# Optimization experiments

Hardware: AMD Instinct MI355X
Metric: run time of the kernel (lower is better)

The kernel has to match this reference:

```python
import jax, jax.numpy as jnp
import numpy as np

Q_SCALE = 64  # 1 << 6, from quantize_8bit default
Q_STEP = 2.0 / Q_SCALE
Q_MIN = -(2 ** 7) / Q_SCALE      # -128/64 = -2.0
Q_MAX = (2 ** 7 - 1) / Q_SCALE   # 127/64


def quantize_8bit(x):
    # round-to-step with straight-through estimator (matches slayer quantize), then clamp
    xq = x + jax.lax.stop_gradient(jnp.round(x / Q_STEP) * Q_STEP - x)
    return jnp.clip(xq, Q_MIN, Q_MAX)


def weight_norm(v, g):
    # per-output-channel weight norm: w = g * v / ||v||  (v: [out, in])
    n = jnp.sqrt(jnp.sum(v * v, axis=1, keepdims=True))
    return g[:, None] * v / n


def sigma_delta_block(x, v, g, clamp6):
    # x: [N, Cin, H, W, T]
    qw = quantize_8bit(weight_norm(v, g))           # [Cout, Cin], 8-bit quantized
    y = jnp.einsum('oi,nihwt->nohwt', qw, x)        # 1x1x1 conv (pointwise)
    s = jnp.cumsum(y, axis=-1)                      # sigma unit: accumulate over time
    mean = jnp.mean(s, axis=(0, 2, 3, 4), keepdims=True)  # mean-only batchnorm
    a = s - mean
    if clamp6:                                      # Clamp6 activation (fc2); Ind = identity (fc1)
        a = jnp.clip(a, -6.0, 6.0)
    # delta unit, threshold=0: d[t] = a[t] - a[t-1], a[-1] = 0
    d = jnp.diff(a, axis=-1, prepend=jnp.zeros_like(a[..., :1]))
    return d


def setup_inputs() -> dict:
    key = jax.random.key(0)
    k = jax.random.split(key, 5)
    N, C, H, W, T = 4, 128, 32, 32, 32
    Cs = 32
    x = jax.random.normal(k[0], (N, C, H, W, T), dtype=jnp.float32)
    v1 = jax.random.normal(k[1], (Cs, C), dtype=jnp.float32) * 0.1
    g1 = jax.random.uniform(k[2], (Cs,), dtype=jnp.float32) + 0.5
    v2 = jax.random.normal(k[3], (C, Cs), dtype=jnp.float32) * 0.1
    g2 = jax.random.uniform(k[4], (C,), dtype=jnp.float32) + 0.5
    return {'x': x, 'v1': v1, 'g1': g1, 'v2': v2, 'g2': g2}


def reference(x, v1, g1, v2, g2):
    h = sigma_delta_block(x, v1, g1, clamp6=False)   # fc1: Ind activation
    out = sigma_delta_block(h, v2, g2, clamp6=True)  # fc2: Clamp6 activation
    return out
```

## Files before the change

kernel.cpp:

```cpp
#include <hip/hip_runtime.h>

#define CIN  128
#define CHUNKF 32768

typedef float f32x4 __attribute__((ext_vector_type(4)));
typedef short s16x8 __attribute__((ext_vector_type(8)));


__device__ __forceinline__ uint pack_hilo(float f) {
  uint b = __float_as_uint(f);
  uint hi = b & 0xffff0000u;
  float lo = f - __uint_as_float(hi);
  return (hi >> 16) | (__float_as_uint(lo) & 0xffff0000u);
}

__global__ __launch_bounds__(256) void wnorm_mean_kernel(
    const float* __restrict__ x,
    const float* __restrict__ v1, const float* __restrict__ g1,
    const float* __restrict__ v2, const float* __restrict__ g2,
    float* __restrict__ ws) {
  int tid = threadIdx.x;
  if (blockIdx.x < 2048) {
    int b = blockIdx.x;
    int chunk = b >> 2, quarter = b & 3;
    int i = chunk & 127;
    const float4* xp = (const float4*)(x + (size_t)chunk * CHUNKF + (size_t)quarter * 8192);
    float acc = 0.f;
#pragma unroll
    for (int it = 0; it < 8; ++it) {
      int f4i = tid + 256 * it;
      float4 v = xp[f4i];
      int t0 = (4 * f4i) & 31;
      acc += v.x * (float)(32 - t0) + v.y * (float)(31 - t0)
           + v.z * (float)(30 - t0) + v.w * (float)(29 - t0);
    }
    for (int off = 32; off >= 1; off >>= 1) acc += __shfl_down(acc, off);
    __shared__ float part[4];
    if ((tid & 63) == 0) part[tid >> 6] = acc;
    __syncthreads();
    if (tid == 0) atomicAdd(&ws[8192 + i], part[0] + part[1] + part[2] + part[3]);
  } else {
    int b = blockIdx.x - 2048;
    bool first = (b < 32);
    int row = first ? b : b - 32;
    int len = first ? 128 : 32;
    const float* v = first ? v1 : v2;
    const float* g = first ? g1 : g2;

    double val = 0.0;
    if (tid < len) { double t = (double)v[row * len + tid]; val = t * t; }
    for (int off = 32; off >= 1; off >>= 1) val += __shfl_down(val, off);
    __shared__ double partial[4];
    if ((tid & 63) == 0) partial[tid >> 6] = val;
    __syncthreads();
    double norm = sqrt(partial[0] + partial[1]);
    if (tid < len) {
      double w = (double)g[row] * (double)v[row * len + tid] / norm;
      double qd = rint(w * 32.0) * 0.03125;
      qd = fmin(fmax(qd, -2.0), 1.984375);
      float qf = (float)qd;
      ushort bf = (ushort)(__float_as_uint(qf) >> 16);
      if (first) {
        ws[row * 128 + tid] = qf;
        ((ushort*)(ws + 8448))[row * 128 + tid] = bf;
      } else {
        ws[4096 + row * 32 + tid] = qf;
        ((ushort*)(ws + 10496))[row * 32 + tid] = bf;
      }
    }
  }
}

__global__ __launch_bounds__(256, 4) void fused_kernel(
    const float* __restrict__ x, const float* __restrict__ ws,
    float* __restrict__ out) {
  const ushort* qw1bf = (const ushort*)(ws + 8448);
  const ushort* qw2bf = (const ushort*)(ws + 10496);

  __shared__ uint xs[8192];
  __shared__ float zred[288];
  __shared__ float kls[128];

  const int tid = threadIdx.x;
  const int wv = tid >> 6;
  const int l  = tid & 63;
  const int g  = l >> 4;
  const int ln = l & 15;

  const int nb  = blockIdx.x >> 8;
  const int hw0 = (blockIdx.x & 255) * 4;
  const float* xblk = x + (size_t)nb * CIN * CHUNKF + (size_t)hw0 * 32;

  float4 xr[8];
#pragma unroll
  for (int k = 0; k < 8; ++k) {
    int f = k * 256 + tid, c = f >> 5, n4 = f & 31;
    xr[k] = *(const float4*)(xblk + (size_t)c * CHUNKF + n4 * 4);
  }

  s16x8 A1[2][4];
#pragma unroll
  for (int jt = 0; jt < 2; ++jt)
#pragma unroll
    for (int ks = 0; ks < 4; ++ks)
      A1[jt][ks] = *(const s16x8*)(qw1bf + (jt * 16 + ln) * 128 + ks * 32 + g * 8);

  {
    int j = tid & 31, grp = tid >> 5;
    const float* qr = ws + j * 128 + grp * 16;
    const float* mr = ws + 8192 + grp * 16;
    float pp = 0.f;
#pragma unroll
    for (int cc = 0; cc < 16; ++cc) pp += qr[cc] * mr[cc];
    zred[j * 8 + grp] = pp;
  }
  __syncthreads();
  if (tid < 32) {
    float t = 0.f;
#pragma unroll
    for (int gg = 0; gg < 8; ++gg) t += zred[tid * 8 + gg];
    zred[256 + tid] = t * (1.0f / 131072.0f);
  }
  __syncthreads();
  if (tid < 128) {
    const float* q2 = ws + 4096 + tid * 32;
    float kk = 0.f;
#pragma unroll 8
    for (int j = 0; j < 32; ++j) kk += q2[j] * zred[256 + j];
    kls[tid] = kk;
  }

  f32x4 acc1[2][2];
#pragma unroll
  for (int a = 0; a < 2; ++a)
#pragma unroll
    for (int b = 0; b < 2; ++b) acc1[a][b] = (f32x4){0.f, 0.f, 0.f, 0.f};

#pragma unroll
  for (int ph = 0; ph < 2; ++ph) {
#pragma unroll
    for (int k = 0; k < 8; ++k) {
      int f = k * 256 + tid, c = f >> 5, n4 = f & 31;
      int u = n4 ^ ((c >> 2) & 6);
      uint4 pk;
      pk.x = pack_hilo(xr[k].x); pk.y = pack_hilo(xr[k].y);
      pk.z = pack_hilo(xr[k].z); pk.w = pack_hilo(xr[k].w);
      *(uint4*)&xs[c * 128 + u * 4] = pk;
    }
    __syncthreads();
    if (ph == 0) {
#pragma unroll
      for (int k = 0; k < 8; ++k) {
        int f = k * 256 + tid, c = f >> 5, n4 = f & 31;
        xr[k] = *(const float4*)(xblk + (size_t)(64 + c) * CHUNKF + n4 * 4);
      }
    }
#pragma unroll
    for (int kl = 0; kl < 2; ++kl) {
#pragma unroll
      for (int nt = 0; nt < 2; ++nt) {
        const int n = wv * 32 + nt * 16 + ln;
        uint q0, q1, q2, q3, q4, q5, q6, q7;
        {
          const int base = (kl * 32 + g * 8) * 128;
          const int u = ((n >> 2) ^ (((kl * 32 + g * 8) >> 2) & 6)) * 4 + (n & 3);
          q0 = xs[base + 0 * 128 + u]; q1 = xs[base + 1 * 128 + u];
          q2 = xs[base + 2 * 128 + u]; q3 = xs[base + 3 * 128 + u];
          q4 = xs[base + 4 * 128 + u]; q5 = xs[base + 5 * 128 + u];
          q6 = xs[base + 6 * 128 + u]; q7 = xs[base + 7 * 128 + u];
        }
        uint4 H, L;
        H.x = (q0 & 0xffffu) | (q1 << 16);  H.y = (q2 & 0xffffu) | (q3 << 16);
        H.z = (q4 & 0xffffu) | (q5 << 16);  H.w = (q6 & 0xffffu) | (q7 << 16);
        L.x = (q0 >> 16) | (q1 & 0xffff0000u); L.y = (q2 >> 16) | (q3 & 0xffff0000u);
        L.z = (q4 >> 16) | (q5 & 0xffff0000u); L.w = (q6 >> 16) | (q7 & 0xffff0000u);
        s16x8 Bh = __builtin_bit_cast(s16x8, H);
        s16x8 Bl = __builtin_bit_cast(s16x8, L);
#pragma unroll
        for (int jt = 0; jt < 2; ++jt) {
          acc1[jt][nt] = __builtin_amdgcn_mfma_f32_16x16x32_bf16(
              A1[jt][ph * 2 + kl], Bh, acc1[jt][nt], 0, 0, 0);
          acc1[jt][nt] = __builtin_amdgcn_mfma_f32_16x16x32_bf16(
              A1[jt][ph * 2 + kl], Bl, acc1[jt][nt], 0, 0, 0);
        }
      }
    }
    __syncthreads();
  }

  uint* zw = xs + wv * 1024;
#pragma unroll
  for (int jt = 0; jt < 2; ++jt)
#pragma unroll
    for (int nt = 0; nt < 2; ++nt) {
      int n = nt * 16 + ln;
      int u = (jt * 4 + g) ^ (n & 7);
      uint4 pk;
      pk.x = pack_hilo(acc1[jt][nt][0]);
      pk.y = pack_hilo(acc1[jt][nt][1]);
      pk.z = pack_hilo(acc1[jt][nt][2]);
      pk.w = pack_hilo(acc1[jt][nt][3]);
      *(uint4*)&zw[n * 32 + u * 4] = pk;
    }

  s16x8 Ah[2], Al[2];
#pragma unroll
  for (int mt = 0; mt < 2; ++mt) {
    int n = mt * 16 + ln;
    int u0 = (2 * g) ^ (n & 7);
    int u1 = (2 * g + 1) ^ (n & 7);
    uint4 qa = *(const uint4*)&zw[n * 32 + u0 * 4];
    uint4 qb = *(const uint4*)&zw[n * 32 + u1 * 4];
    uint4 H, L;
    H.x = (qa.x & 0xffffu) | (qa.y << 16);  H.y = (qa.z & 0xffffu) | (qa.w << 16);
    H.z = (qb.x & 0xffffu) | (qb.y << 16);  H.w = (qb.z & 0xffffu) | (qb.w << 16);
    L.x = (qa.x >> 16) | (qa.y & 0xffff0000u); L.y = (qa.z >> 16) | (qa.w & 0xffff0000u);
    L.z = (qb.x >> 16) | (qb.y & 0xffff0000u); L.w = (qb.z >> 16) | (qb.w & 0xffff0000u);
    Ah[mt] = __builtin_bit_cast(s16x8, H);
    Al[mt] = __builtin_bit_cast(s16x8, L);
  }

  const size_t outbase = (size_t)nb * CIN * CHUNKF + (size_t)(hw0 + wv) * 32;
#pragma unroll 1
  for (int h = 0; h < 2; ++h) {
    s16x8 B2[4];
#pragma unroll
    for (int q = 0; q < 4; ++q)
      B2[q] = *(const s16x8*)(qw2bf + ((h * 4 + q) * 16 + ln) * 32 + g * 8);

    f32x4 acc2[4][2];
#pragma unroll
    for (int a = 0; a < 4; ++a)
#pragma unroll
      for (int b = 0; b < 2; ++b) acc2[a][b] = (f32x4){0.f, 0.f, 0.f, 0.f};

#pragma unroll
    for (int mt = 0; mt < 2; ++mt)
#pragma unroll
      for (int q = 0; q < 4; ++q) {
        acc2[q][mt] = __builtin_amdgcn_mfma_f32_16x16x32_bf16(Ah[mt], B2[q], acc2[q][mt], 0, 0, 0);
        acc2[q][mt] = __builtin_amdgcn_mfma_f32_16x16x32_bf16(Al[mt], B2[q], acc2[q][mt], 0, 0, 0);
      }

#pragma unroll
    for (int q = 0; q < 4; ++q) {
      const int nt = h * 4 + q;
      float c0[2], c1[2], c2[2], c3[2], base[2], Qi0 = 0.f;
#pragma unroll
      for (int mt = 0; mt < 2; ++mt) {
        c0[mt] = acc2[q][mt][0];
        c1[mt] = c0[mt] + acc2[q][mt][1];
        c2[mt] = c1[mt] + acc2[q][mt][2];
        c3[mt] = c2[mt] + acc2[q][mt][3];
        float Qi = c3[mt];
        float t1 = __shfl_up(Qi, 16); if (g >= 1) Qi += t1;
        float t2 = __shfl_up(Qi, 32); if (g >= 2) Qi += t2;
        base[mt] = Qi - c3[mt];
        if (mt == 0) Qi0 = Qi;
      }
      float S0tot = __shfl(Qi0, 48 + ln);
      base[1] += S0tot;
      const float kpp = kls[nt * 16 + ln];
      float* op = out + outbase + (size_t)(nt * 16 + ln) * CHUNKF;
#pragma unroll
      for (int mt = 0; mt < 2; ++mt) {
        float Bv = base[mt] - kpp;
        float prev = fminf(fmaxf(Bv, -6.f), 6.f);
        if (mt == 0 && g == 0) prev = 0.f;
        float A0 = fminf(fmaxf(Bv + c0[mt], -6.f), 6.f);
        float A1v = fminf(fmaxf(Bv + c1[mt], -6.f), 6.f);
        float A2v = fminf(fmaxf(Bv + c2[mt], -6.f), 6.f);
        float A3v = fminf(fmaxf(Bv + c3[mt], -6.f), 6.f);
        *(float4*)(op + mt * 16 + g * 4) =
            make_float4(A0 - prev, A1v - A0, A2v - A1v, A3v - A2v);
      }
    }
  }
}

extern "C" void kernel_launch(void* const* d_in, const int* in_sizes, int n_in,
                              void* d_out, int out_size, void* d_ws, size_t ws_size,
                              hipStream_t stream) {
  const float* x  = (const float*)d_in[0];
  const float* v1 = (const float*)d_in[1];
  const float* g1 = (const float*)d_in[2];
  const float* v2 = (const float*)d_in[3];
  const float* g2 = (const float*)d_in[4];
  float* ws  = (float*)d_ws;
  float* out = (float*)d_out;

  hipMemsetAsync(ws + 8192, 0, 128 * sizeof(float), stream);
  wnorm_mean_kernel<<<2208, 256, 0, stream>>>(x, v1, g1, v2, g2, ws);
  fused_kernel<<<1024, 256, 0, stream>>>(x, ws, out);
}
```

Measured before the change: 49.39 us.

## Fuse weight-norm, mean reduction and main pass into one cooperative kernel

Adds a cooperative kernel with 512 persistent blocks that first computes the time-weighted channel sums of its own x slice into 32 sharded atomic slots and quantizes the weights, then does a grid-wide sync and runs the two-GEMM sigma-delta pass over two 4-position groups, prefetching the next group's x into registers. It removes the separate pre-pass kernel launch and spreads the atomic contention across slots. In exchange it adds per-launch host queries for device attributes and occupancy, a grid barrier, and reads x twice within the same kernel. The old two-kernel path remains as a fallback when cooperative launch or the needed occupancy is unavailable.

Result: no change. 49.28 us (-0.2%).

```diff
diff --git a/kernel.cpp b/kernel.cpp
--- a/kernel.cpp
+++ b/kernel.cpp
@@ -1,4 +1,7 @@
 #include <hip/hip_runtime.h>
+#include <hip/hip_cooperative_groups.h>
+
+namespace cg = cooperative_groups;
 
 #define CIN  128
 #define CHUNKF 32768
@@ -46,7 +49,6 @@
     int len = first ? 128 : 32;
     const float* v = first ? v1 : v2;
     const float* g = first ? g1 : g2;
-
     double val = 0.0;
     if (tid < len) { double t = (double)v[row * len + tid]; val = t * t; }
     for (int off = 32; off >= 1; off >>= 1) val += __shfl_down(val, off);
@@ -160,15 +162,12 @@
 #pragma unroll
       for (int nt = 0; nt < 2; ++nt) {
         const int n = wv * 32 + nt * 16 + ln;
-        uint q0, q1, q2, q3, q4, q5, q6, q7;
-        {
-          const int base = (kl * 32 + g * 8) * 128;
-          const int u = ((n >> 2) ^ (((kl * 32 + g * 8) >> 2) & 6)) * 4 + (n & 3);
-          q0 = xs[base + 0 * 128 + u]; q1 = xs[base + 1 * 128 + u];
-          q2 = xs[base + 2 * 128 + u]; q3 = xs[base + 3 * 128 + u];
-          q4 = xs[base + 4 * 128 + u]; q5 = xs[base + 5 * 128 + u];
-          q6 = xs[base + 6 * 128 + u]; q7 = xs[base + 7 * 128 + u];
-        }
+        const int base = (kl * 32 + g * 8) * 128;
+        const int u = ((n >> 2) ^ (((kl * 32 + g * 8) >> 2) & 6)) * 4 + (n & 3);
+        uint q0 = xs[base + 0 * 128 + u], q1 = xs[base + 1 * 128 + u];
+        uint q2 = xs[base + 2 * 128 + u], q3 = xs[base + 3 * 128 + u];
+        uint q4 = xs[base + 4 * 128 + u], q5 = xs[base + 5 * 128 + u];
+        uint q6 = xs[base + 6 * 128 + u], q7 = xs[base + 7 * 128 + u];
         uint4 H, L;
         H.x = (q0 & 0xffffu) | (q1 << 16);  H.y = (q2 & 0xffffu) | (q3 << 16);
         H.z = (q4 & 0xffffu) | (q5 << 16);  H.w = (q6 & 0xffffu) | (q7 << 16);
@@ -178,10 +177,8 @@
         s16x8 Bl = __builtin_bit_cast(s16x8, L);
 #pragma unroll
         for (int jt = 0; jt < 2; ++jt) {
-          acc1[jt][nt] = __builtin_amdgcn_mfma_f32_16x16x32_bf16(
-              A1[jt][ph * 2 + kl], Bh, acc1[jt][nt], 0, 0, 0);
-          acc1[jt][nt] = __builtin_amdgcn_mfma_f32_16x16x32_bf16(
-              A1[jt][ph * 2 + kl], Bl, acc1[jt][nt], 0, 0, 0);
+          acc1[jt][nt] = __builtin_amdgcn_mfma_f32_16x16x32_bf16(A1[jt][ph * 2 + kl], Bh, acc1[jt][nt], 0, 0, 0);
+          acc1[jt][nt] = __builtin_amdgcn_mfma_f32_16x16x32_bf16(A1[jt][ph * 2 + kl], Bl, acc1[jt][nt], 0, 0, 0);
         }
       }
     }
@@ -227,13 +224,11 @@
 #pragma unroll
     for (int q = 0; q < 4; ++q)
       B2[q] = *(const s16x8*)(qw2bf + ((h * 4 + q) * 16 + ln) * 32 + g * 8);
-
     f32x4 acc2[4][2];
 #pragma unroll
     for (int a = 0; a < 4; ++a)
 #pragma unroll
       for (int b = 0; b < 2; ++b) acc2[a][b] = (f32x4){0.f, 0.f, 0.f, 0.f};
-
 #pragma unroll
     for (int mt = 0; mt < 2; ++mt)
 #pragma unroll
@@ -241,7 +236,6 @@
         acc2[q][mt] = __builtin_amdgcn_mfma_f32_16x16x32_bf16(Ah[mt], B2[q], acc2[q][mt], 0, 0, 0);
         acc2[q][mt] = __builtin_amdgcn_mfma_f32_16x16x32_bf16(Al[mt], B2[q], acc2[q][mt], 0, 0, 0);
       }
-
 #pragma unroll
     for (int q = 0; q < 4; ++q) {
       const int nt = h * 4 + q;
@@ -278,6 +272,288 @@
   }
 }
 
+__global__ __launch_bounds__(256, 2) void fused_all(
+    const float* __restrict__ x,
+    const float* __restrict__ v1, const float* __restrict__ g1,
+    const float* __restrict__ v2, const float* __restrict__ g2,
+    float* __restrict__ ws, float* __restrict__ out) {
+  __shared__ uint xs[8192];
+  __shared__ float mls[128];
+  __shared__ float zred[256];
+  __shared__ float zsm[32];
+  __shared__ float kls[128];
+  __shared__ double wpart[4];
+
+  const int tid = threadIdx.x;
+  const int bid = blockIdx.x;
+  const int nb  = bid >> 7;
+  const int hw8 = (bid & 127) * 8;
+  float* msumP = ws + 8192;
+
+  {
+    const int l63 = tid & 63, wvp = tid >> 6;
+    const int t0 = (4 * l63) & 31;
+    const float wt0 = (float)(32 - t0), wt1 = (float)(31 - t0);
+    const float wt2 = (float)(30 - t0), wt3 = (float)(29 - t0);
+    const int slot = bid & 31;
+    const float* xsl = x + (size_t)nb * CIN * CHUNKF + (size_t)hw8 * 32 + l63 * 4;
+#pragma unroll 4
+    for (int k = 0; k < 32; ++k) {
+      int c = k * 4 + wvp;
+      float4 v = *(const float4*)(xsl + (size_t)c * CHUNKF);
+      float pv = v.x * wt0 + v.y * wt1 + v.z * wt2 + v.w * wt3;
+      pv += __shfl_down(pv, 32);
+      pv += __shfl_down(pv, 16);
+      pv += __shfl_down(pv, 8);
+      pv += __shfl_down(pv, 4);
+      pv += __shfl_down(pv, 2);
+      pv += __shfl_down(pv, 1);
+      if (l63 == 0) atomicAdd(&msumP[slot * 128 + c], pv);
+    }
+  }
+
+  if (bid < 160) {
+    bool first = (bid < 32);
+    int row = first ? bid : bid - 32;
+    int len = first ? 128 : 32;
+    const float* v = first ? v1 : v2;
+    const float* g = first ? g1 : g2;
+    double val = 0.0;
+    if (tid < len) { double t = (double)v[row * len + tid]; val = t * t; }
+    for (int off = 32; off >= 1; off >>= 1) val += __shfl_down(val, off);
+    if ((tid & 63) == 0) wpart[tid >> 6] = val;
+    __syncthreads();
+    double norm = sqrt(wpart[0] + wpart[1]);
+    if (tid < len) {
+      double w = (double)g[row] * (double)v[row * len + tid] / norm;
+      double qd = rint(w * 32.0) * 0.03125;
+      qd = fmin(fmax(qd, -2.0), 1.984375);
+      float qf = (float)qd;
+      ushort bf = (ushort)(__float_as_uint(qf) >> 16);
+      if (first) {
+        ws[row * 128 + tid] = qf;
+        ((ushort*)(ws + 12544))[row * 128 + tid] = bf;
+      } else {
+        ws[4096 + row * 32 + tid] = qf;
+        ((ushort*)(ws + 14592))[row * 32 + tid] = bf;
+      }
+    }
+  }
+
+  cg::this_grid().sync();
+
+  const ushort* qw1bf = (const ushort*)(ws + 12544);
+  const ushort* qw2bf = (const ushort*)(ws + 14592);
+  const int wv = tid >> 6;
+  const int l  = tid & 63;
+  const int g  = l >> 4;
+  const int ln = l & 15;
+
+  s16x8 A1[2][4];
+#pragma unroll
+  for (int jt = 0; jt < 2; ++jt)
+#pragma unroll
+    for (int ks = 0; ks < 4; ++ks)
+      A1[jt][ks] = *(const s16x8*)(qw1bf + (jt * 16 + ln) * 128 + ks * 32 + g * 8);
+
+  float4 xr[8];
+  {
+    const float* xg = x + (size_t)nb * CIN * CHUNKF + (size_t)hw8 * 32;
+#pragma unroll
+    for (int k = 0; k < 8; ++k) {
+      int f = k * 256 + tid, c = f >> 5, n4 = f & 31;
+      xr[k] = *(const float4*)(xg + (size_t)c * CHUNKF + n4 * 4);
+    }
+  }
+
+  if (tid < 128) {
+    float m = 0.f;
+#pragma unroll
+    for (int p = 0; p < 32; ++p) m += msumP[p * 128 + tid];
+    mls[tid] = m;
+  }
+  __syncthreads();
+  {
+    int j = tid & 31, grp8 = tid >> 5;
+    const float* qr = ws + j * 128 + grp8 * 16;
+    float pp = 0.f;
+#pragma unroll
+    for (int cc = 0; cc < 16; ++cc) pp += qr[cc] * mls[grp8 * 16 + cc];
+    zred[j * 8 + grp8] = pp;
+  }
+  __syncthreads();
+  if (tid < 32) {
+    float t = 0.f;
+#pragma unroll
+    for (int gg = 0; gg < 8; ++gg) t += zred[tid * 8 + gg];
+    zsm[tid] = t * (1.0f / 131072.0f);
+  }
+  __syncthreads();
+  if (tid < 128) {
+    const float* q2p = ws + 4096 + tid * 32;
+    float kk = 0.f;
+#pragma unroll 8
+    for (int j = 0; j < 32; ++j) kk += q2p[j] * zsm[j];
+    kls[tid] = kk;
+  }
+
+#pragma unroll 1
+  for (int grp = 0; grp < 2; ++grp) {
+    const int hw0 = hw8 + grp * 4;
+    const float* xg = x + (size_t)nb * CIN * CHUNKF + (size_t)hw0 * 32;
+
+    f32x4 acc1[2][2];
+#pragma unroll
+    for (int a = 0; a < 2; ++a)
+#pragma unroll
+      for (int b = 0; b < 2; ++b) acc1[a][b] = (f32x4){0.f, 0.f, 0.f, 0.f};
+
+    __syncthreads();
+
+#pragma unroll
+    for (int ph = 0; ph < 2; ++ph) {
+#pragma unroll
+      for (int k = 0; k < 8; ++k) {
+        int f = k * 256 + tid, c = f >> 5, n4 = f & 31;
+        int u = n4 ^ ((c >> 2) & 6);
+        uint4 pk;
+        pk.x = pack_hilo(xr[k].x); pk.y = pack_hilo(xr[k].y);
+        pk.z = pack_hilo(xr[k].z); pk.w = pack_hilo(xr[k].w);
+        *(uint4*)&xs[c * 128 + u * 4] = pk;
+      }
+      __syncthreads();
+      if (ph == 0) {
+#pragma unroll
+        for (int k = 0; k < 8; ++k) {
+          int f = k * 256 + tid, c = f >> 5, n4 = f & 31;
+          xr[k] = *(const float4*)(xg + (size_t)(64 + c) * CHUNKF + n4 * 4);
+        }
+      }
+#pragma unroll
+      for (int kl = 0; kl < 2; ++kl) {
+#pragma unroll
+        for (int nt = 0; nt < 2; ++nt) {
+          const int n = wv * 32 + nt * 16 + ln;
+          const int base = (kl * 32 + g * 8) * 128;
+          const int u = ((n >> 2) ^ (((kl * 32 + g * 8) >> 2) & 6)) * 4 + (n & 3);
+          uint q0 = xs[base + 0 * 128 + u], q1 = xs[base + 1 * 128 + u];
+          uint q2 = xs[base + 2 * 128 + u], q3 = xs[base + 3 * 128 + u];
+          uint q4 = xs[base + 4 * 128 + u], q5 = xs[base + 5 * 128 + u];
+          uint q6 = xs[base + 6 * 128 + u], q7 = xs[base + 7 * 128 + u];
+          uint4 H, L;
+          H.x = (q0 & 0xffffu) | (q1 << 16);  H.y = (q2 & 0xffffu) | (q3 << 16);
+          H.z = (q4 & 0xffffu) | (q5 << 16);  H.w = (q6 & 0xffffu) | (q7 << 16);
+          L.x = (q0 >> 16) | (q1 & 0xffff0000u); L.y = (q2 >> 16) | (q3 & 0xffff0000u);
+          L.z = (q4 >> 16) | (q5 & 0xffff0000u); L.w = (q6 >> 16) | (q7 & 0xffff0000u);
+          s16x8 Bh = __builtin_bit_cast(s16x8, H);
+          s16x8 Bl = __builtin_bit_cast(s16x8, L);
+#pragma unroll
+          for (int jt = 0; jt < 2; ++jt) {
+            acc1[jt][nt] = __builtin_amdgcn_mfma_f32_16x16x32_bf16(A1[jt][ph * 2 + kl], Bh, acc1[jt][nt], 0, 0, 0);
+            acc1[jt][nt] = __builtin_amdgcn_mfma_f32_16x16x32_bf16(A1[jt][ph * 2 + kl], Bl, acc1[jt][nt], 0, 0, 0);
+          }
+        }
+      }
+      __syncthreads();
+    }
+
+    uint* zw = xs + wv * 1024;
+#pragma unroll
+    for (int jt = 0; jt < 2; ++jt)
+#pragma unroll
+      for (int nt = 0; nt < 2; ++nt) {
+        int n = nt * 16 + ln;
+        int u = (jt * 4 + g) ^ (n & 7);
+        uint4 pk;
+        pk.x = pack_hilo(acc1[jt][nt][0]);
+        pk.y = pack_hilo(acc1[jt][nt][1]);
+        pk.z = pack_hilo(acc1[jt][nt][2]);
+        pk.w = pack_hilo(acc1[jt][nt][3]);
+        *(uint4*)&zw[n * 32 + u * 4] = pk;
+      }
+
+    s16x8 Ah[2], Al[2];
+#pragma unroll
+    for (int mt = 0; mt < 2; ++mt) {
+      int n = mt * 16 + ln;
+      int u0 = (2 * g) ^ (n & 7);
+      int u1 = (2 * g + 1) ^ (n & 7);
+      uint4 qa = *(const uint4*)&zw[n * 32 + u0 * 4];
+      uint4 qb = *(const uint4*)&zw[n * 32 + u1 * 4];
+      uint4 H, L;
+      H.x = (qa.x & 0xffffu) | (qa.y << 16);  H.y = (qa.z & 0xffffu) | (qa.w << 16);
+      H.z = (qb.x & 0xffffu) | (qb.y << 16);  H.w = (qb.z & 0xffffu) | (qb.w << 16);
+      L.x = (qa.x >> 16) | (qa.y & 0xffff0000u); L.y = (qa.z >> 16) | (qa.w & 0xffff0000u);
+      L.z = (qb.x >> 16) | (qb.y & 0xffff0000u); L.w = (qb.z >> 16) | (qb.w & 0xffff0000u);
+      Ah[mt] = __builtin_bit_cast(s16x8, H);
+      Al[mt] = __builtin_bit_cast(s16x8, L);
+    }
+
+    if (grp == 0) {
+      const float* xg1 = x + (size_t)nb * CIN * CHUNKF + (size_t)(hw8 + 4) * 32;
+#pragma unroll
+      for (int k = 0; k < 8; ++k) {
+        int f = k * 256 + tid, c = f >> 5, n4 = f & 31;
+        xr[k] = *(const float4*)(xg1 + (size_t)c * CHUNKF + n4 * 4);
+      }
+    }
+
+    const size_t outbase = (size_t)nb * CIN * CHUNKF + (size_t)(hw0 + wv) * 32;
+#pragma unroll 1
+    for (int h = 0; h < 2; ++h) {
+      s16x8 B2[4];
+#pragma unroll
+      for (int q = 0; q < 4; ++q)
+        B2[q] = *(const s16x8*)(qw2bf + ((h * 4 + q) * 16 + ln) * 32 + g * 8);
+      f32x4 acc2[4][2];
+#pragma unroll
+      for (int a = 0; a < 4; ++a)
+#pragma unroll
+        for (int b = 0; b < 2; ++b) acc2[a][b] = (f32x4){0.f, 0.f, 0.f, 0.f};
+#pragma unroll
+      for (int mt = 0; mt < 2; ++mt)
+#pragma unroll
+        for (int q = 0; q < 4; ++q) {
+          acc2[q][mt] = __builtin_amdgcn_mfma_f32_16x16x32_bf16(Ah[mt], B2[q], acc2[q][mt], 0, 0, 0);
+          acc2[q][mt] = __builtin_amdgcn_mfma_f32_16x16x32_bf16(Al[mt], B2[q], acc2[q][mt], 0, 0, 0);
+        }
+#pragma unroll
+      for (int q = 0; q < 4; ++q) {
+        const int nt = h * 4 + q;
+        float c0[2], c1[2], c2[2], c3[2], base[2], Qi0 = 0.f;
+#pragma unroll
+        for (int mt = 0; mt < 2; ++mt) {
+          c0[mt] = acc2[q][mt][0];
+          c1[mt] = c0[mt] + acc2[q][mt][1];
+          c2[mt] = c1[mt] + acc2[q][mt][2];
+          c3[mt] = c2[mt] + acc2[q][mt][3];
+          float Qi = c3[mt];
+          float t1 = __shfl_up(Qi, 16); if (g >= 1) Qi += t1;
+          float t2 = __shfl_up(Qi, 32); if (g >= 2) Qi += t2;
+          base[mt] = Qi - c3[mt];
+          if (mt == 0) Qi0 = Qi;
+        }
+        float S0tot = __shfl(Qi0, 48 + ln);
+        base[1] += S0tot;
+        const float kpp = kls[nt * 16 + ln];
+        float* op = out + outbase + (size_t)(nt * 16 + ln) * CHUNKF;
+#pragma unroll
+        for (int mt = 0; mt < 2; ++mt) {
+          float Bv = base[mt] - kpp;
+          float prev = fminf(fmaxf(Bv, -6.f), 6.f);
+          if (mt == 0 && g == 0) prev = 0.f;
+          float A0 = fminf(fmaxf(Bv + c0[mt], -6.f), 6.f);
+          float A1v = fminf(fmaxf(Bv + c1[mt], -6.f), 6.f);
+          float A2v = fminf(fmaxf(Bv + c2[mt], -6.f), 6.f);
+          float A3v = fminf(fmaxf(Bv + c3[mt], -6.f), 6.f);
+          *(float4*)(op + mt * 16 + g * 4) =
+              make_float4(A0 - prev, A1v - A0, A2v - A1v, A3v - A2v);
+        }
+      }
+    }
+  }
+}
+
 extern "C" void kernel_launch(void* const* d_in, const int* in_sizes, int n_in,
                               void* d_out, int out_size, void* d_ws, size_t ws_size,
                               hipStream_t stream) {
@@ -289,7 +565,21 @@
   float* ws  = (float*)d_ws;
   float* out = (float*)d_out;
 
-  hipMemsetAsync(ws + 8192, 0, 128 * sizeof(float), stream);
+  hipMemsetAsync(ws + 8192, 0, 4096 * sizeof(float), stream);
+
+  int dev = 0, coop = 0, occ = 0;
+  hipGetDevice(&dev);
+  hipDeviceGetAttribute(&coop, hipDeviceAttributeCooperativeLaunch, dev);
+  hipOccupancyMaxActiveBlocksPerMultiprocessor(&occ, fused_all, 256, 0);
+
+  if (coop && occ >= 2) {
+    void* args[] = { (void*)&x, (void*)&v1, (void*)&g1, (void*)&v2, (void*)&g2,
+                     (void*)&ws, (void*)&out };
+    hipError_t e = hipLaunchCooperativeKernel((const void*)fused_all, dim3(512),
+                                              dim3(256), args, 0, stream);
+    if (e == hipSuccess) return;
+  }
+
   wnorm_mean_kernel<<<2208, 256, 0, stream>>>(x, v1, g1, v2, g2, ws);
   fused_kernel<<<1024, 256, 0, stream>>>(x, ws, out);
 }
```

## Process two spatial tiles per block and prefetch the next tile's input

Applied to the files above, without the earlier changes.

The fused kernel now handles 8 spatial positions per block in two iterations instead of 4, halving the grid to 512 blocks. During the second phase of the first tile it issues global loads for the next tile's first channel half, overlapping them with the first GEMM and second-stage work. The per-block prologue (weight fragment loads, mean/kls reduction) is amortized over twice the work. The cost is fewer blocks on a large GPU, which may leave CUs underfilled, plus an extra barrier per tile.

After: 63.05 us. +27.7%, slower.

```diff
diff --git a/kernel.cpp b/kernel.cpp
--- a/kernel.cpp
+++ b/kernel.cpp
@@ -46,7 +46,6 @@
     int len = first ? 128 : 32;
     const float* v = first ? v1 : v2;
     const float* g = first ? g1 : g2;
-
     double val = 0.0;
     if (tid < len) { double t = (double)v[row * len + tid]; val = t * t; }
     for (int off = 32; off >= 1; off >>= 1) val += __shfl_down(val, off);
@@ -87,15 +86,15 @@
   const int g  = l >> 4;
   const int ln = l & 15;
 
-  const int nb  = blockIdx.x >> 8;
-  const int hw0 = (blockIdx.x & 255) * 4;
-  const float* xblk = x + (size_t)nb * CIN * CHUNKF + (size_t)hw0 * 32;
+  const int nb   = blockIdx.x >> 7;
+  const int pos8 = (blockIdx.x & 127) * 8;
+  const float* xblk0 = x + (size_t)nb * CIN * CHUNKF + (size_t)pos8 * 32;
 
   float4 xr[8];
 #pragma unroll
   for (int k = 0; k < 8; ++k) {
     int f = k * 256 + tid, c = f >> 5, n4 = f & 31;
-    xr[k] = *(const float4*)(xblk + (size_t)c * CHUNKF + n4 * 4);
+    xr[k] = *(const float4*)(xblk0 + (size_t)c * CHUNKF + n4 * 4);
   }
 
   s16x8 A1[2][4];
@@ -130,149 +129,153 @@
     kls[tid] = kk;
   }
 
-  f32x4 acc1[2][2];
-#pragma unroll
-  for (int a = 0; a < 2; ++a)
-#pragma unroll
-    for (int b = 0; b < 2; ++b) acc1[a][b] = (f32x4){0.f, 0.f, 0.f, 0.f};
-
-#pragma unroll
-  for (int ph = 0; ph < 2; ++ph) {
-#pragma unroll
-    for (int k = 0; k < 8; ++k) {
-      int f = k * 256 + tid, c = f >> 5, n4 = f & 31;
-      int u = n4 ^ ((c >> 2) & 6);
-      uint4 pk;
-      pk.x = pack_hilo(xr[k].x); pk.y = pack_hilo(xr[k].y);
-      pk.z = pack_hilo(xr[k].z); pk.w = pack_hilo(xr[k].w);
-      *(uint4*)&xs[c * 128 + u * 4] = pk;
-    }
-    __syncthreads();
-    if (ph == 0) {
+#pragma unroll 1
+  for (int it = 0; it < 2; ++it) {
+    const float* xblk = xblk0 + it * 128;
+
+    f32x4 acc1[2][2];
+#pragma unroll
+    for (int a = 0; a < 2; ++a)
+#pragma unroll
+      for (int b = 0; b < 2; ++b) acc1[a][b] = (f32x4){0.f, 0.f, 0.f, 0.f};
+
+#pragma unroll
+    for (int ph = 0; ph < 2; ++ph) {
 #pragma unroll
       for (int k = 0; k < 8; ++k) {
         int f = k * 256 + tid, c = f >> 5, n4 = f & 31;
-        xr[k] = *(const float4*)(xblk + (size_t)(64 + c) * CHUNKF + n4 * 4);
-      }
-    }
-#pragma unroll
-    for (int kl = 0; kl < 2; ++kl) {
-#pragma unroll
-      for (int nt = 0; nt < 2; ++nt) {
-        const int n = wv * 32 + nt * 16 + ln;
-        uint q0, q1, q2, q3, q4, q5, q6, q7;
-        {
+        int u = n4 ^ ((c >> 2) & 6);
+        uint4 pk;
+        pk.x = pack_hilo(xr[k].x); pk.y = pack_hilo(xr[k].y);
+        pk.z = pack_hilo(xr[k].z); pk.w = pack_hilo(xr[k].w);
+        *(uint4*)&xs[c * 128 + u * 4] = pk;
+      }
+      __syncthreads();
+      if (ph == 0) {
+#pragma unroll
+        for (int k = 0; k < 8; ++k) {
+          int f = k * 256 + tid, c = f >> 5, n4 = f & 31;
+          xr[k] = *(const float4*)(xblk + (size_t)(64 + c) * CHUNKF + n4 * 4);
+        }
+      } else if (it == 0) {
+#pragma unroll
+        for (int k = 0; k < 8; ++k) {
+          int f = k * 256 + tid, c = f >> 5, n4 = f & 31;
+          xr[k] = *(const float4*)(xblk0 + 128 + (size_t)c * CHUNKF + n4 * 4);
+        }
+      }
+#pragma unroll
+      for (int kl = 0; kl < 2; ++kl) {
+#pragma unroll
+        for (int nt = 0; nt < 2; ++nt) {
+          const int n = wv * 32 + nt * 16 + ln;
           const int base = (kl * 32 + g * 8) * 128;
           const int u = ((n >> 2) ^ (((kl * 32 + g * 8) >> 2) & 6)) * 4 + (n & 3);
-          q0 = xs[base + 0 * 128 + u]; q1 = xs[base + 1 * 128 + u];
-          q2 = xs[base + 2 * 128 + u]; q3 = xs[base + 3 * 128 + u];
-          q4 = xs[base + 4 * 128 + u]; q5 = xs[base + 5 * 128 + u];
-          q6 = xs[base + 6 * 128 + u]; q7 = xs[base + 7 * 128 + u];
-        }
-        uint4 H, L;
-        H.x = (q0 & 0xffffu) | (q1 << 16);  H.y = (q2 & 0xffffu) | (q3 << 16);
-        H.z = (q4 & 0xffffu) | (q5 << 16);  H.w = (q6 & 0xffffu) | (q7 << 16);
-        L.x = (q0 >> 16) | (q1 & 0xffff0000u); L.y = (q2 >> 16) | (q3 & 0xffff0000u);
-        L.z = (q4 >> 16) | (q5 & 0xffff0000u); L.w = (q6 >> 16) | (q7 & 0xffff0000u);
-        s16x8 Bh = __builtin_bit_cast(s16x8, H);
-        s16x8 Bl = __builtin_bit_cast(s16x8, L);
-#pragma unroll
-        for (int jt = 0; jt < 2; ++jt) {
-          acc1[jt][nt] = __builtin_amdgcn_mfma_f32_16x16x32_bf16(
-              A1[jt][ph * 2 + kl], Bh, acc1[jt][nt], 0, 0, 0);
-          acc1[jt][nt] = __builtin_amdgcn_mfma_f32_16x16x32_bf16(
-              A1[jt][ph * 2 + kl], Bl, acc1[jt][nt], 0, 0, 0);
-        }
-      }
+          uint q0 = xs[base + 0 * 128 + u], q1 = xs[base + 1 * 128 + u];
+          uint q2 = xs[base + 2 * 128 + u], q3 = xs[base + 3 * 128 + u];
+          uint q4 = xs[base + 4 * 128 + u], q5 = xs[base + 5 * 128 + u];
+          uint q6 = xs[base + 6 * 128 + u], q7 = xs[base + 7 * 128 + u];
+          uint4 H, L;
+          H.x = (q0 & 0xffffu) | (q1 << 16);  H.y = (q2 & 0xffffu) | (q3 << 16);
+          H.z = (q4 & 0xffffu) | (q5 << 16);  H.w = (q6 & 0xffffu) | (q7 << 16);
+          L.x = (q0 >> 16) | (q1 & 0xffff0000u); L.y = (q2 >> 16) | (q3 & 0xffff0000u);
+          L.z = (q4 >> 16) | (q5 & 0xffff0000u); L.w = (q6 >> 16) | (q7 & 0xffff0000u);
+          s16x8 Bh = __builtin_bit_cast(s16x8, H);
+          s16x8 Bl = __builtin_bit_cast(s16x8, L);
+#pragma unroll
+          for (int jt = 0; jt < 2; ++jt) {
+            acc1[jt][nt] = __builtin_amdgcn_mfma_f32_16x16x32_bf16(A1[jt][ph * 2 + kl], Bh, acc1[jt][nt], 0, 0, 0);
+            acc1[jt][nt] = __builtin_amdgcn_mfma_f32_16x16x32_bf16(A1[jt][ph * 2 + kl], Bl, acc1[jt][nt], 0, 0, 0);
+          }
+        }
+      }
+      __syncthreads();
+    }
+
+    uint* zw = xs + wv * 1024;
+#pragma unroll
+    for (int jt = 0; jt < 2; ++jt)
+#pragma unroll
+      for (int nt = 0; nt < 2; ++nt) {
+        int n = nt * 16 + ln;
+        int u = (jt * 4 + g) ^ (n & 7);
+        uint4 pk;
+        pk.x = pack_hilo(acc1[jt][nt][0]);
+        pk.y = pack_hilo(acc1[jt][nt][1]);
+        pk.z = pack_hilo(acc1[jt][nt][2]);
+        pk.w = pack_hilo(acc1[jt][nt][3]);
+        *(uint4*)&zw[n * 32 + u * 4] = pk;
+      }
+
+    s16x8 Ah[2], Al[2];
+#pragma unroll
+    for (int mt = 0; mt < 2; ++mt) {
+      int n = mt * 16 + ln;
+      int u0 = (2 * g) ^ (n & 7);
+      int u1 = (2 * g + 1) ^ (n & 7);
+      uint4 qa = *(const uint4*)&zw[n * 32 + u0 * 4];
+      uint4 qb = *(const uint4*)&zw[n * 32 + u1 * 4];
+      uint4 H, L;
+      H.x = (qa.x & 0xffffu) | (qa.y << 16);  H.y = (qa.z & 0xffffu) | (qa.w << 16);
+      H.z = (qb.x & 0xffffu) | (qb.y << 16);  H.w = (qb.z & 0xffffu) | (qb.w << 16);
+      L.x = (qa.x >> 16) | (qa.y & 0xffff0000u); L.y = (qa.z >> 16) | (qa.w & 0xffff0000u);
+      L.z = (qb.x >> 16) | (qb.y & 0xffff0000u); L.w = (qb.z >> 16) | (qb.w & 0xffff0000u);
+      Ah[mt] = __builtin_bit_cast(s16x8, H);
+      Al[mt] = __builtin_bit_cast(s16x8, L);
     }
     __syncthreads();
-  }
-
-  uint* zw = xs + wv * 1024;
-#pragma unroll
-  for (int jt = 0; jt < 2; ++jt)
-#pragma unroll
-    for (int nt = 0; nt < 2; ++nt) {
-      int n = nt * 16 + ln;
-      int u = (jt * 4 + g) ^ (n & 7);
-      uint4 pk;
-      pk.x = pack_hilo(acc1[jt][nt][0]);
-      pk.y = pack_hilo(acc1[jt][nt][1]);
-      pk.z = pack_hilo(acc1[jt][nt][2]);
-      pk.w = pack_hilo(acc1[jt][nt][3]);
-      *(uint4*)&zw[n * 32 + u * 4] = pk;
-    }
-
-  s16x8 Ah[2], Al[2];
-#pragma unroll
-  for (int mt = 0; mt < 2; ++mt) {
-    int n = mt * 16 + ln;
-    int u0 = (2 * g) ^ (n & 7);
-    int u1 = (2 * g + 1) ^ (n & 7);
-    uint4 qa = *(const uint4*)&zw[n * 32 + u0 * 4];
-    uint4 qb = *(const uint4*)&zw[n * 32 + u1 * 4];
-    uint4 H, L;
-    H.x = (qa.x & 0xffffu) | (qa.y << 16);  H.y = (qa.z & 0xffffu) | (qa.w << 16);
-    H.z = (qb.x & 0xffffu) | (qb.y << 16);  H.w = (qb.z & 0xffffu) | (qb.w << 16);
-    L.x = (qa.x >> 16) | (qa.y & 0xffff0000u); L.y = (qa.z >> 16) | (qa.w & 0xffff0000u);
-    L.z = (qb.x >> 16) | (qb.y & 0xffff0000u); L.w = (qb.z >> 16) | (qb.w & 0xffff0000u);
-    Ah[mt] = __builtin_bit_cast(s16x8, H);
-    Al[mt] = __builtin_bit_cast(s16x8, L);
-  }
-
-  const size_t outbase = (size_t)nb * CIN * CHUNKF + (size_t)(hw0 + wv) * 32;
+
+    const size_t outbase = (size_t)nb * CIN * CHUNKF + (size_t)(pos8 + it * 4 + wv) * 32;
 #pragma unroll 1
-  for (int h = 0; h < 2; ++h) {
-    s16x8 B2[4];
-#pragma unroll
-    for (int q = 0; q < 4; ++q)
-      B2[q] = *(const s16x8*)(qw2bf + ((h * 4 + q) * 16 + ln) * 32 + g * 8);
-
-    f32x4 acc2[4][2];
-#pragma unroll
-    for (int a = 0; a < 4; ++a)
-#pragma unroll
-      for (int b = 0; b < 2; ++b) acc2[a][b] = (f32x4){0.f, 0.f, 0.f, 0.f};
-
-#pragma unroll
-    for (int mt = 0; mt < 2; ++mt)
+    for (int h = 0; h < 2; ++h) {
+      s16x8 B2[4];
+#pragma unroll
+      for (int q = 0; q < 4; ++q)
+        B2[q] = *(const s16x8*)(qw2bf + ((h * 4 + q) * 16 + ln) * 32 + g * 8);
+      f32x4 acc2[4][2];
+#pragma unroll
+      for (int a = 0; a < 4; ++a)
+#pragma unroll
+        for (int b = 0; b < 2; ++b) acc2[a][b] = (f32x4){0.f, 0.f, 0.f, 0.f};
+#pragma unroll
+      for (int mt = 0; mt < 2; ++mt)
+#pragma unroll
+        for (int q = 0; q < 4; ++q) {
+          acc2[q][mt] = __builtin_amdgcn_mfma_f32_16x16x32_bf16(Ah[mt], B2[q], acc2[q][mt], 0, 0, 0);
+          acc2[q][mt] = __builtin_amdgcn_mfma_f32_16x16x32_bf16(Al[mt], B2[q], acc2[q][mt], 0, 0, 0);
+        }
 #pragma unroll
       for (int q = 0; q < 4; ++q) {
-        acc2[q][mt] = __builtin_amdgcn_mfma_f32_16x16x32_bf16(Ah[mt], B2[q], acc2[q][mt], 0, 0, 0);
-        acc2[q][mt] = __builtin_amdgcn_mfma_f32_16x16x32_bf16(Al[mt], B2[q], acc2[q][mt], 0, 0, 0);
-      }
-
-#pragma unroll
-    for (int q = 0; q < 4; ++q) {
-      const int nt = h * 4 + q;
-      float c0[2], c1[2], c2[2], c3[2], base[2], Qi0 = 0.f;
-#pragma unroll
-      for (int mt = 0; mt < 2; ++mt) {
-        c0[mt] = acc2[q][mt][0];
-        c1[mt] = c0[mt] + acc2[q][mt][1];
-        c2[mt] = c1[mt] + acc2[q][mt][2];
-        c3[mt] = c2[mt] + acc2[q][mt][3];
-        float Qi = c3[mt];
-        float t1 = __shfl_up(Qi, 16); if (g >= 1) Qi += t1;
-        float t2 = __shfl_up(Qi, 32); if (g >= 2) Qi += t2;
-        base[mt] = Qi - c3[mt];
-        if (mt == 0) Qi0 = Qi;
-      }
-      float S0tot = __shfl(Qi0, 48 + ln);
-      base[1] += S0tot;
-      const float kpp = kls[nt * 16 + ln];
-      float* op = out + outbase + (size_t)(nt * 16 + ln) * CHUNKF;
-#pragma unroll
-      for (int mt = 0; mt < 2; ++mt) {
-        float Bv = base[mt] - kpp;
-        float prev = fminf(fmaxf(Bv, -6.f), 6.f);
-        if (mt == 0 && g == 0) prev = 0.f;
-        float A0 = fminf(fmaxf(Bv + c0[mt], -6.f), 6.f);
-        float A1v = fminf(fmaxf(Bv + c1[mt], -6.f), 6.f);
-        float A2v = fminf(fmaxf(Bv + c2[mt], -6.f), 6.f);
-        float A3v = fminf(fmaxf(Bv + c3[mt], -6.f), 6.f);
-        *(float4*)(op + mt * 16 + g * 4) =
-            make_float4(A0 - prev, A1v - A0, A2v - A1v, A3v - A2v);
+        const int nt = h * 4 + q;
+        float c0[2], c1[2], c2[2], c3[2], base[2], Qi0 = 0.f;
+#pragma unroll
+        for (int mt = 0; mt < 2; ++mt) {
+          c0[mt] = acc2[q][mt][0];
+          c1[mt] = c0[mt] + acc2[q][mt][1];
+          c2[mt] = c1[mt] + acc2[q][mt][2];
+          c3[mt] = c2[mt] + acc2[q][mt][3];
+          float Qi = c3[mt];
+          float t1 = __shfl_up(Qi, 16); if (g >= 1) Qi += t1;
+          float t2 = __shfl_up(Qi, 32); if (g >= 2) Qi += t2;
+          base[mt] = Qi - c3[mt];
+          if (mt == 0) Qi0 = Qi;
+        }
+        float S0tot = __shfl(Qi0, 48 + ln);
+        base[1] += S0tot;
+        const float kpp = kls[nt * 16 + ln];
+        float* op = out + outbase + (size_t)(nt * 16 + ln) * CHUNKF;
+#pragma unroll
+        for (int mt = 0; mt < 2; ++mt) {
+          float Bv = base[mt] - kpp;
+          float prev = fminf(fmaxf(Bv, -6.f), 6.f);
+          if (mt == 0 && g == 0) prev = 0.f;
+          float A0 = fminf(fmaxf(Bv + c0[mt], -6.f), 6.f);
+          float A1v = fminf(fmaxf(Bv + c1[mt], -6.f), 6.f);
+          float A2v = fminf(fmaxf(Bv + c2[mt], -6.f), 6.f);
+          float A3v = fminf(fmaxf(Bv + c3[mt], -6.f), 6.f);
+          *(float4*)(op + mt * 16 + g * 4) =
+              make_float4(A0 - prev, A1v - A0, A2v - A1v, A3v - A2v);
+        }
       }
     }
   }
@@ -291,5 +294,5 @@
 
   hipMemsetAsync(ws + 8192, 0, 128 * sizeof(float), stream);
   wnorm_mean_kernel<<<2208, 256, 0, stream>>>(x, v1, g1, v2, g2, ws);
-  fused_kernel<<<1024, 256, 0, stream>>>(x, ws, out);
-}
+  fused_kernel<<<512, 256, 0, stream>>>(x, ws, out);
+}
```
